# Performance work log

Hardware: AMD Instinct MI355X
Metric: run time of the kernel (lower is better)

## Reference

```python
import jax, jax.numpy as jnp
import numpy as np
import math

N = 1500; E = 24000; C_IN = 16; H = 64; NUM_LAYERS = 10; RATIO = 0.9
NEG = -1e9


def setup_inputs() -> dict:
    key = jax.random.key(0)
    ks = jax.random.split(key, 40)
    it = iter(range(40))
    def nrm(shape, scale=0.1):
        return jax.random.normal(ks[next(it)], shape, dtype=jnp.float32) * scale
    src = jax.random.randint(ks[next(it)], (E,), 0, N, dtype=jnp.int32)
    off = jax.random.randint(ks[next(it)], (E,), 1, N, dtype=jnp.int32)
    dst = (src + off) % N  # no self loops in the raw edge list
    return dict(
        x=nrm((N, C_IN), 1.0),
        edge_src=src, edge_dst=dst,
        W1=nrm((C_IN, H // 2)), b1=jnp.zeros((H // 2,), jnp.float32),
        W2=nrm((H // 2, H)), b2=jnp.zeros((H,), jnp.float32),
        W3=nrm((H, H)), b3=jnp.zeros((H,), jnp.float32),
        Wrel=nrm((NUM_LAYERS - 1, H, H)), brel=jnp.zeros((NUM_LAYERS - 1, H), jnp.float32),
        Wroot=nrm((NUM_LAYERS - 1, H, H)),
        pW=nrm((4, H, H)), pb=jnp.zeros((4, H), jnp.float32),
        leW1=nrm((4, H, 1)), leb1=jnp.zeros((4, 1), jnp.float32),
        leW2=nrm((4, H, 1)),
        leW3=nrm((4, H, 1)), leb3=jnp.zeros((4, 1), jnp.float32),
        linW1=nrm((NUM_LAYERS * H, H)), linb1=jnp.zeros((H,), jnp.float32),
        linW2=nrm((H, 10)), linb2=jnp.zeros((10,), jnp.float32),
    )


def _seg_mean(vals, idx, n):
    s = jax.ops.segment_sum(vals, idx, num_segments=n)
    c = jax.ops.segment_sum(jnp.ones((idx.shape[0],), vals.dtype), idx, num_segments=n)
    return s / jnp.maximum(c, 1.0)[:, None]


def _feast(x, W, b, srcL, dstL, n):
    # FeaStConv with heads=1: softmax over a single head == 1 -> mean of lin(x_j) + bias
    return _seg_mean((x @ W)[srcL], dstL, n) + b


def _gconv_sparse(x, src, dst, Wr, br, Wo, n):
    return _seg_mean(x[src], dst, n) @ Wr + br + x @ Wo


def _gconv_dense(x, A, Wr, br, Wo):
    # mean aggregation: divide weighted sum by count of (nonzero) in-edges
    Mf = (A != 0).astype(x.dtype)
    agg = (A.T @ x) / jnp.maximum(Mf.sum(0), 1.0)[:, None]
    return agg @ Wr + br + x @ Wo


def _topk_pool(xc, fitness, ratio):
    k = int(math.ceil(ratio * xc.shape[0]))
    fit_k, perm = jax.lax.top_k(fitness, k)
    return xc[perm] * fit_k[:, None], perm


def _asap_sparse(x, src, dst, pW, pb, leW1, leb1, leW2, leW3, leb3):
    n = x.shape[0]
    ar = jnp.arange(n, dtype=src.dtype)
    srcL = jnp.concatenate([src, ar])  # add remaining self loops (weight 1)
    dstL = jnp.concatenate([dst, ar])
    xq = jax.ops.segment_max(x[srcL], dstL, num_segments=n) @ pW + pb
    s = jax.nn.leaky_relu(jnp.sum(xq[dstL] * x[srcL], -1), 0.2)
    m = jax.ops.segment_max(s, dstL, num_segments=n)
    e = jnp.exp(s - m[dstL])
    score = e / jax.ops.segment_sum(e, dstL, num_segments=n)[dstL]
    xc = jax.ops.segment_sum(x[srcL] * score[:, None], dstL, num_segments=n)
    # LEConv fitness score (edge weight = 1)
    a = xc @ leW1 + leb1
    b = xc @ leW2
    agg = jax.ops.segment_sum(a[srcL] - b[dstL], dstL, num_segments=n)
    fitness = jax.nn.sigmoid((agg + xc @ leW3 + leb3)[:, 0])
    x_new, perm = _topk_pool(xc, fitness, RATIO)
    S = jnp.zeros((n, n), x.dtype).at[srcL, dstL].add(score)
    A = jnp.zeros((n, n), x.dtype).at[srcL, dstL].add(1.0)
    Sp = S[:, perm]
    A_new = Sp.T @ A @ Sp
    k = A_new.shape[0]
    return x_new, A_new * (1.0 - jnp.eye(k, dtype=x.dtype))  # remove diag


def _asap_dense(x, A, pW, pb, leW1, leb1, leW2, leW3, leb3):
    n = x.shape[0]
    A = A + jnp.diag((jnp.diag(A) == 0).astype(A.dtype))  # add remaining self loops
    M = A != 0
    Mf = M.astype(x.dtype)
    xq = jnp.max(jnp.where(M[:, :, None], x[:, None, :], NEG), axis=0) @ pW + pb  # [n,H]
    Sc = jnp.where(M, jax.nn.leaky_relu(x @ xq.T, 0.2), NEG)  # [j,i]
    m = Sc.max(0)
    e = jnp.where(M, jnp.exp(Sc - m), 0.0)
    score = e / e.sum(0)
    xc = score.T @ x
    a = xc @ leW1 + leb1
    b = xc @ leW2
    agg = Mf.T @ a - Mf.sum(0)[:, None] * b
    fitness = jax.nn.sigmoid((agg + xc @ leW3 + leb3)[:, 0])
    x_new, perm = _topk_pool(xc, fitness, RATIO)
    Sp = score[:, perm]
    A_new = Sp.T @ A @ Sp
    k = A_new.shape[0]
    return x_new, A_new * (1.0 - jnp.eye(k, dtype=x.dtype))


def _forward(x, edge_src, edge_dst, W1, b1, W2, b2, W3, b3, Wrel, brel, Wroot,
             pW, pb, leW1, leb1, leW2, leW3, leb3, linW1, linb1, linW2, linb2):
    n = x.shape[0]
    ar = jnp.arange(n, dtype=edge_src.dtype)
    srcL = jnp.concatenate([edge_src, ar])  # FeaStConv add_self_loops=True
    dstL = jnp.concatenate([edge_dst, ar])
    x = jax.nn.elu(_feast(x, W1, b1, srcL, dstL, n))
    x = jax.nn.elu(_feast(x, W2, b2, srcL, dstL, n))
    x = jax.nn.elu(_feast(x, W3, b3, srcL, dstL, n))
    xs = [x.mean(0, keepdims=True)]  # single graph -> global_mean_pool == mean
    A = None
    for i in range(NUM_LAYERS - 1):
        if A is None:
            x = jax.nn.relu(_gconv_sparse(x, edge_src, edge_dst, Wrel[i], brel[i], Wroot[i], x.shape[0]))
        else:
            x = jax.nn.relu(_gconv_dense(x, A, Wrel[i], brel[i], Wroot[i]))
        xs.append(x.mean(0, keepdims=True))
        if i % 2 == 0 and i < NUM_LAYERS - 2:
            p = i // 2
            args = (pW[p], pb[p], leW1[p], leb1[p], leW2[p], leW3[p], leb3[p])
            if A is None:
                x, A = _asap_sparse(x, edge_src, edge_dst, *args)
            else:
                x, A = _asap_dense(x, A, *args)
    h = jnp.concatenate(xs, axis=-1)  # [1, NUM_LAYERS*H] jumping-knowledge cat
    h = jax.nn.relu(h @ linW1 + linb1)
    return jax.nn.log_softmax(h @ linW2 + linb2, axis=-1)


def reference(x, edge_src, edge_dst, W1, b1, W2, b2, W3, b3, Wrel, brel, Wroot,
              pW, pb, leW1, leb1, leW2, leW3, leb3, linW1, linb1, linW2, linb2):
    return _forward(x, edge_src, edge_dst, W1, b1, W2, b2, W3, b3, Wrel, brel, Wroot,
                    pW, pb, leW1, leb1, leW2, leW3, leb3, linW1, linb1, linW2, linb2)
```

## Files before the change

kernel.cpp:

```cpp
#include <hip/hip_runtime.h>
#include <math.h>

#define NEGV -1000000000.0f

typedef short short8 __attribute__((ext_vector_type(8)));
typedef float floatx4 __attribute__((ext_vector_type(4)));

__device__ __forceinline__ float sigm(float x){ return 1.0f/(1.0f+expf(-x)); }
__device__ __forceinline__ void edge_sd(int e,const int* src,const int* dst,int E,int& s,int& d){
  if(e<E){ s=src[e]; d=dst[e]; } else { s=e-E; d=s; }
}
__device__ __forceinline__ ushort bf16rn(float x){
  unsigned u = __float_as_uint(x);
  unsigned r = (u + 0x7fffu + ((u>>16)&1u)) >> 16;
  return (ushort)r;
}
__device__ __forceinline__ float bf16f(ushort h){ return __uint_as_float(((unsigned)h)<<16); }

__global__ void k_zero(float* __restrict__ p, size_t n){
  size_t i = (size_t)blockIdx.x*256 + threadIdx.x;
  if (i < n) p[i] = 0.0f;
}
__global__ void k_fillm1(int* __restrict__ p, int n){
  int i = blockIdx.x*256 + threadIdx.x;
  if (i < n) p[i] = -1;
}
__global__ void k_ipos(const int* __restrict__ perm, int* __restrict__ ipos, int kk){
  int p = blockIdx.x*256 + threadIdx.x;
  if (p < kk) ipos[perm[p]] = p;
}
__global__ void k_prep2(const int* __restrict__ rowD,const int* __restrict__ eidD,
                        const float* __restrict__ scE,int2* __restrict__ Mt,int L2,int kk){
  int p = blockIdx.x*256+threadIdx.x; if(p>=L2) return;
  Mt[p] = make_int2(rowD[p]*kk, __float_as_int(scE[eidD[p]]));
}

__global__ void k_split3(const float* __restrict__ src,int R,int Cs,int ld,
                         ushort* __restrict__ dst,int Cp,int bmode){
  int idx = blockIdx.x*256+threadIdx.x;
  if (idx >= R*Cp) return;
  int r = idx / Cp, c = idx - r*Cp;
  float x = (c < Cs) ? src[(size_t)r*ld + c] : 0.0f;
  ushort h = bf16rn(x);
  ushort l = bf16rn(x - bf16f(h));
  size_t base = (size_t)r*(3*Cp) + c;
  dst[base]        = h;
  dst[base + Cp]   = bmode ? l : h;
  dst[base + 2*Cp] = bmode ? h : l;
}
__global__ void k_split3_Tdual(const float* __restrict__ src,int Rs,int Cs,int ld,
                               const int* __restrict__ gperm,const float* __restrict__ cscale,
                               const float* __restrict__ emax,
                               ushort* __restrict__ dstA,ushort* __restrict__ dstB,
                               ushort* __restrict__ dstCpad,int Kp){
  __shared__ float t[32][33];
  int tx = threadIdx.x & 31, ty = threadIdx.x >> 5;
  int kb = blockIdx.y*32, xb = blockIdx.x*32;
  int x = xb + tx;
  int gx = (x < Cs) ? gperm[x] : 0;
#pragma unroll
  for (int i=0;i<4;i++){
    int k = kb + ty + i*8;
    t[ty+i*8][tx] = (k < Rs && x < Cs) ? src[(size_t)k*ld + gx] : 0.0f;
  }
  __syncthreads();
  const int K3 = 3*Kp;
#pragma unroll
  for (int i=0;i<4;i++){
    int xo = xb + ty + i*8, ko = kb + tx;
    if (xo < Cs){
      float v = 0.0f;
      if (ko < Rs){
        int g = gperm[xo];
        v = expf(t[tx][ty+i*8] - emax[g]) * cscale[g];
      }
      ushort h = bf16rn(v);
      ushort l = bf16rn(v - bf16f(h));
      size_t base = (size_t)xo*K3 + ko;
      dstA[base] = h; dstA[base+Kp] = h; dstA[base+2*Kp] = l;
      dstB[base] = h; dstB[base+Kp] = l; dstB[base+2*Kp] = h;
      if (ko >= Rs){ dstCpad[base]=0; dstCpad[base+Kp]=0; dstCpad[base+2*Kp]=0; }
    }
  }
}

template<int EPI>
__global__ __launch_bounds__(256) void k_gemm_mfma(
    const ushort* __restrict__ A, const ushort* __restrict__ B,
    float* __restrict__ C, int ldc, int M, int N, int K3,
    const float* __restrict__ mask, int ldm)
{
  __shared__ ushort As[2][64][72];
  __shared__ ushort Bs[2][64][72];
  const int tid = threadIdx.x;
  const int m0 = blockIdx.y*64, n0 = blockIdx.x*64;
  const int w = tid>>6, lane = tid&63;
  const int lo4 = lane&15, quad = lane>>4;
  const int sr = tid>>2, sseg = tid&3;

  floatx4 acc[4];
#pragma unroll
  for(int c=0;c<4;c++){ acc[c][0]=0.f; acc[c][1]=0.f; acc[c][2]=0.f; acc[c][3]=0.f; }

  const size_t arow = (size_t)(m0+sr)*K3;
  const size_t brow = (size_t)(n0+sr)*K3;
  const bool aval = (m0+sr) < M;
  const bool bval = (n0+sr) < N;

  uint4 av0 = make_uint4(0,0,0,0), av1 = make_uint4(0,0,0,0);
  uint4 bv0 = make_uint4(0,0,0,0), bv1 = make_uint4(0,0,0,0);
  if (aval){ av0 = *(const uint4*)(A + arow + sseg*8);
             av1 = *(const uint4*)(A + arow + 32 + sseg*8); }
  if (bval){ bv0 = *(const uint4*)(B + brow + sseg*8);
             bv1 = *(const uint4*)(B + brow + 32 + sseg*8); }
  *(uint4*)&As[0][sr][sseg*8] = av0; *(uint4*)&As[0][sr][32+sseg*8] = av1;
  *(uint4*)&Bs[0][sr][sseg*8] = bv0; *(uint4*)&Bs[0][sr][32+sseg*8] = bv1;
  __syncthreads();

  const int T = K3 >> 6;
  for (int i=0;i<T;i++){
    const int cb = i & 1;
    if (i+1 < T){
      const int k0 = (i+1)<<6;
      av0 = make_uint4(0,0,0,0); av1 = make_uint4(0,0,0,0);
      bv0 = make_uint4(0,0,0,0); bv1 = make_uint4(0,0,0,0);
      if (aval){ av0 = *(const uint4*)(A + arow + k0 + sseg*8);
                 av1 = *(const uint4*)(A + arow + k0 + 32 + sseg*8); }
      if (bval){ bv0 = *(const uint4*)(B + brow + k0 + sseg*8);
                 bv1 = *(const uint4*)(B + brow + k0 + 32 + sseg*8); }
    }
    short8 af0 = *(const short8*)&As[cb][16*w + lo4][quad*8];
    short8 af1 = *(const short8*)&As[cb][16*w + lo4][32+quad*8];
#pragma unroll
    for (int c=0;c<4;c++){
      short8 bf0 = *(const short8*)&Bs[cb][16*c + lo4][quad*8];
      acc[c] = __builtin_amdgcn_mfma_f32_16x16x32_bf16(af0, bf0, acc[c], 0, 0, 0);
      short8 bf1 = *(const short8*)&Bs[cb][16*c + lo4][32+quad*8];
      acc[c] = __builtin_amdgcn_mfma_f32_16x16x32_bf16(af1, bf1, acc[c], 0, 0, 0);
    }
    if (i+1 < T){
      __syncthreads();
      *(uint4*)&As[1-cb][sr][sseg*8] = av0; *(uint4*)&As[1-cb][sr][32+sseg*8] = av1;
      *(uint4*)&Bs[1-cb][sr][sseg*8] = bv0; *(uint4*)&Bs[1-cb][sr][32+sseg*8] = bv1;
      __syncthreads();
    }
  }

#pragma unroll
  for (int c=0;c<4;c++){
    const int gn = n0 + 16*c + lo4;
#pragma unroll
    for (int r=0;r<4;r++){
      const int gm = m0 + 16*w + quad*4 + r;
      if (gm < M && gn < N){
        float v = acc[c][r];
        if (EPI==1) v = (mask[(size_t)gm*ldm+gn] != 0.0f || gm==gn) ? (v > 0.0f ? v : 0.2f*v) : NEGV;
        C[(size_t)gm*ldc+gn] = v;
      }
    }
  }
}

__global__ __launch_bounds__(256) void k_gemm_pp(
    const ushort* __restrict__ A, const ushort* __restrict__ B,
    float* __restrict__ P0, float* __restrict__ P1,
    float* __restrict__ P2, float* __restrict__ P3, int ldp,
    int M, int N, int K3, int kchunk)
{
  __shared__ ushort As[2][128][72];
  __shared__ ushort Bs[2][128][72];
  const int tid = threadIdx.x;
  const int m0 = blockIdx.y*128, n0 = blockIdx.x*128;
  const int w = tid>>6, lane = tid&63;
  const int lo4 = lane&15, quad = lane>>4;
  const int wr = w>>1, wc = w&1;

  const int srow = tid>>1, shalf = tid&1;

  const int z = blockIdx.z;
  float* __restrict__ P = (z==0) ? P0 : (z==1) ? P1 : (z==2) ? P2 : P3;
  const int kbeg = z * kchunk;
  int klen = K3 - kbeg; if (klen > kchunk) klen = kchunk; if (klen < 0) klen = 0;
  const int T = klen >> 6;

  floatx4 acc[4][4];
#pragma unroll
  for(int i=0;i<4;i++)
#pragma unroll
    for(int c=0;c<4;c++){ acc[i][c][0]=0.f; acc[i][c][1]=0.f; acc[i][c][2]=0.f; acc[i][c][3]=0.f; }

  const size_t arow = (size_t)(m0+srow)*K3 + kbeg + shalf*32;
  const size_t brow = (size_t)(n0+srow)*K3 + kbeg + shalf*32;
  const bool aval = (m0+srow) < M;
  const bool bval = (n0+srow) < N;
  const int sbase = shalf*32;

  uint4 apre[4], bpre[4];
#pragma unroll
  for(int s=0;s<4;s++){ apre[s]=make_uint4(0,0,0,0); bpre[s]=make_uint4(0,0,0,0); }
  if (aval){
#pragma unroll
    for(int s=0;s<4;s++) apre[s] = *(const uint4*)(A + arow + s*8);
  }
  if (bval){
#pragma unroll
    for(int s=0;s<4;s++) bpre[s] = *(const uint4*)(B + brow + s*8);
  }
#pragma unroll
  for(int s=0;s<4;s++){
    *(uint4*)&As[0][srow][sbase + s*8] = apre[s];
    *(uint4*)&Bs[0][srow][sbase + s*8] = bpre[s];
  }
  __syncthreads();

  for (int it=0; it<T; ++it){
    const int cb = it & 1;
    if (it+1 < T){
      const int k0 = (it+1)<<6;
#pragma unroll
      for(int s=0;s<4;s++){ apre[s]=make_uint4(0,0,0,0); bpre[s]=make_uint4(0,0,0,0); }
      if (aval){
#pragma unroll
        for(int s=0;s<4;s++) apre[s] = *(const uint4*)(A + arow + k0 + s*8);
      }
      if (bval){
#pragma unroll
        for(int s=0;s<4;s++) bpre[s] = *(const uint4*)(B + brow + k0 + s*8);
      }
    }
    short8 af[4][2];
#pragma unroll
    for(int i=0;i<4;i++){
      af[i][0] = *(const short8*)&As[cb][wr*64 + 16*i + lo4][quad*8];
      af[i][1] = *(const short8*)&As[cb][wr*64 + 16*i + lo4][32 + quad*8];
    }
#pragma unroll
    for(int c=0;c<4;c++){
      short8 bf0 = *(const short8*)&Bs[cb][wc*64 + 16*c + lo4][quad*8];
      short8 bf1 = *(const short8*)&Bs[cb][wc*64 + 16*c + lo4][32 + quad*8];
#pragma unroll
      for(int i=0;i<4;i++){
        acc[i][c] = __builtin_amdgcn_mfma_f32_16x16x32_bf16(af[i][0], bf0, acc[i][c], 0, 0, 0);
        acc[i][c] = __builtin_amdgcn_mfma_f32_16x16x32_bf16(af[i][1], bf1, acc[i][c], 0, 0, 0);
      }
    }
    if (it+1 < T){
      __syncthreads();
#pragma unroll
      for(int s=0;s<4;s++){
        *(uint4*)&As[1-cb][srow][sbase + s*8] = apre[s];
        *(uint4*)&Bs[1-cb][srow][sbase + s*8] = bpre[s];
      }
      __syncthreads();
    }
  }

#pragma unroll
  for(int c=0;c<4;c++){
    const int gn = n0 + wc*64 + 16*c + lo4;
    if (gn < N){
#pragma unroll
      for(int i=0;i<4;i++){
#pragma unroll
        for(int r=0;r<4;r++){
          const int gm = m0 + wr*64 + 16*i + quad*4 + r;
          if (gm < M) P[(size_t)gm*ldp+gn] = acc[i][c][r];
        }
      }
    }
  }
}

__global__ __launch_bounds__(256) void k_red_tb(
    const float* __restrict__ P0,const float* __restrict__ P1,
    const float* __restrict__ P2,const float* __restrict__ P3,int ldp,
    const ushort* __restrict__ Bb, ushort* __restrict__ Cb,
    int M,int N,int Kp)
{
  __shared__ float t[32][33];
  const int tx = threadIdx.x & 31, ty = threadIdx.x >> 5;
  const int mb = blockIdx.y*32, nb = blockIdx.x*32;
  const int n = nb + tx;
#pragma unroll
  for (int i=0;i<4;i++){
    int m = mb + ty + i*8;
    float v = 0.0f;
    if (m < M && n < N){
      size_t o = (size_t)m*ldp + n;
      v = (P0[o] + P1[o]) + (P2[o] + P3[o]);
    }
    t[ty+i*8][tx] = v;
  }
  __syncthreads();
  const int K3o = 3*Kp;
#pragma unroll
  for (int i=0;i<4;i++){
    int no = nb + ty + i*8, mo = mb + tx;
    if (no < N && mo < M){
      size_t base = (size_t)no*K3o + mo;
      float sp = bf16f(Bb[base]) + bf16f(Bb[base+Kp]);
      float v = t[tx][ty+i*8] + sp;
      ushort h = bf16rn(v), l = bf16rn(v - bf16f(h));
      Cb[base] = h; Cb[base+Kp] = l; Cb[base+2*Kp] = h;
    }
  }
}

__global__ void k_red_diag(const float* __restrict__ P0,const float* __restrict__ P1,
                           const float* __restrict__ P2,const float* __restrict__ P3,
                           float* __restrict__ C,int kk){
  int idx = blockIdx.x*256+threadIdx.x;
  if (idx >= kk*kk) return;
  int u = idx/kk, v = idx - u*kk;
  float s = (P0[idx] + P1[idx]) + (P2[idx] + P3[idx]);
  C[idx] = (u==v) ? 0.0f : s;
}

template<bool MAXM, bool COUNT, bool EXPM, bool SELF>
__global__ __launch_bounds__(256) void k_skinny(
    const float* __restrict__ A, int lda,
    const float* __restrict__ X,
    const float* __restrict__ mcol,
    float* __restrict__ P, int* __restrict__ cntp,
    int M, int K, int kchunk)
{
  __shared__ float As[16][68];
  __shared__ float Xs[16][68];
  const int tid = threadIdx.x;
  const int m0 = blockIdx.y * 64;
  const int tmb = (tid & 15) * 4, tnb = (tid >> 4) * 4;
  float acc[4][4];
  int cacc[4] = {0,0,0,0};
#pragma unroll
  for (int i=0;i<4;i++)
#pragma unroll
    for (int j=0;j<4;j++) acc[i][j] = MAXM ? NEGV : 0.0f;

  const int kstart = blockIdx.z * kchunk;
  int kend = kstart + kchunk; if (kend > K) kend = K;
  const int ml = tid & 63, tb = tid >> 6;
  const bool mvalid = (m0 + ml) < M;
  float mc = 0.0f;
  if (EXPM && mvalid) mc = mcol[m0 + ml];

  for (int k0 = kstart; k0 < kend; k0 += 16) {
#pragma unroll
    for (int s=0;s<4;s++) {
      const int tk = tb + s*4;
      float va = 0.0f, vx = 0.0f;
      if ((k0+tk) < K) {
        if (mvalid){
          va = A[(size_t)(k0+tk)*lda + m0 + ml];
          if (EXPM) va = expf(va - mc);
        }
        vx = X[(size_t)(k0+tk)*64 + ml];
      }
      As[tk][ml] = va;
      Xs[tk][ml] = vx;
    }
    __syncthreads();
#pragma unroll
    for (int kk=0; kk<16; kk++) {
      const float4 a4 = *(const float4*)&As[kk][tmb];
      const float4 b4 = *(const float4*)&Xs[kk][tnb];
      const float av[4] = {a4.x,a4.y,a4.z,a4.w};
      const float bv[4] = {b4.x,b4.y,b4.z,b4.w};
#pragma unroll
      for (int i=0;i<4;i++){
        if (COUNT) cacc[i] += (av[i] != 0.0f) ? 1 : 0;
#pragma unroll
        for (int j=0;j<4;j++) {
          if (MAXM) acc[i][j] = fmaxf(acc[i][j], av[i] != 0.0f ? bv[j] : NEGV);
          else      acc[i][j] = fmaf(av[i], bv[j], acc[i][j]);
        }
      }
    }
    __syncthreads();
  }

  const size_t slab = (size_t)blockIdx.z * M * 64;
#pragma unroll
  for (int i=0;i<4;i++){
    const int m = m0 + tmb + i;
    if (m < M){
#pragma unroll
      for (int j=0;j<4;j++){
        float v = acc[i][j];
        if (SELF) v = fmaxf(v, X[(size_t)m*64 + tnb + j]);
        P[slab + (size_t)m*64 + tnb + j] = v;
      }
    }
  }
  if (COUNT && tnb == 0){
#pragma unroll
    for (int i=0;i<4;i++){
      const int m = m0 + tmb + i;
      if (m < M) cntp[blockIdx.z*M + m] = cacc[i];
    }
  }
}

__global__ __launch_bounds__(256) void k_poolq(
    const float* __restrict__ SEGP,const int* __restrict__ cntp8,int Z,
    const float* __restrict__ pWp,const float* __restrict__ pbp,
    const float* __restrict__ X,
    ushort* __restrict__ dstA,ushort* __restrict__ dstB,
    float* __restrict__ cntP,int n)
{
  __shared__ float xq[4][65];
  const int tid = threadIdx.x;
  const int r = tid>>6, j = tid&63;
  const int i = blockIdx.x*4 + r;
  float v = NEGV;
  if (i < n){
    for(int z=0;z<Z;z++) v = fmaxf(v, SEGP[(size_t)z*n*64 + (size_t)i*64 + j]);
    if (j == 0){
      int c=1; for(int z=0;z<Z;z++) c += cntp8[z*n+i];
      cntP[i] = (float)c;
    }
  }
  xq[r][j] = v;
  __syncthreads();
  if (i < n){
    float s = pbp[j];
    for(int q=0;q<64;q++) s = fmaf(xq[r][q], pWp[q*64+j], s);
    size_t base = (size_t)i*192 + j;
    ushort h = bf16rn(s), l = bf16rn(s - bf16f(h));
    dstB[base] = h; dstB[base+64] = l; dstB[base+128] = h;
    float x = X[(size_t)i*64 + j];
    h = bf16rn(x); l = bf16rn(x - bf16f(h));
    dstA[base] = h; dstA[base+64] = h; dstA[base+128] = l;
  }
}

__global__ __launch_bounds__(256) void k_gconv_fuse(
    const float* __restrict__ SEGP,const int* __restrict__ cntp8,int Z,
    const float* __restrict__ Wrel,const float* __restrict__ brel,
    const float* __restrict__ X,const float* __restrict__ Wroot,
    float* __restrict__ XN,int n,float* __restrict__ meanacc,float inv_n)
{
  __shared__ float agg_s[4][65];
  __shared__ float xrow[4][65];
  __shared__ float cnt_s[4];
  const int tid = threadIdx.x;
  const int r = tid>>6, j = tid&63;
  const int i = blockIdx.x*4 + r;
  float a = 0.0f;
  if (i < n){
    for(int z=0;z<Z;z++) a += SEGP[(size_t)z*n*64 + (size_t)i*64 + j];
    xrow[r][j] = X[(size_t)i*64 + j];
    if (j == 0){
      int c=0; for(int z=0;z<Z;z++) c += cntp8[z*n+i];
      cnt_s[r] = (float)(c>1?c:1);
    }
  }
  agg_s[r][j] = a;
  __syncthreads();
  float v = 0.0f;
  if (i < n){
    float acc=0.0f, rt=0.0f;
    for(int q=0;q<64;q++){
      acc = fmaf(agg_s[r][q], Wrel[q*64+j], acc);
      rt  = fmaf(xrow[r][q],  Wroot[q*64+j], rt);
    }
    v = fmaxf(acc/cnt_s[r] + brel[j] + rt, 0.0f);
    XN[(size_t)i*64 + j] = v;
  }
  __syncthreads();
  agg_s[r][j] = v;
  __syncthreads();
  if (r == 0) atomicAdd(&meanacc[j], (agg_s[0][j]+agg_s[1][j]+agg_s[2][j]+agg_s[3][j])*inv_n);
}

__global__ __launch_bounds__(256) void k_smax_fused(const float* __restrict__ S,int n,
                                                    float* __restrict__ mcol,float* __restrict__ invd){
  __shared__ float red[16][17];
  const int jc = threadIdx.x & 15, rg = threadIdx.x >> 4;
  const int j = blockIdx.x*16 + jc;
  float m = -3.0e38f;
  if (j < n)
    for(int i=rg;i<n;i+=16) m = fmaxf(m, S[(size_t)i*n+j]);
  red[rg][jc] = m;
  __syncthreads();
  for(int s=8;s>0;s>>=1){
    if(rg<s) red[rg][jc] = fmaxf(red[rg][jc], red[rg+s][jc]);
    __syncthreads();
  }
  const float mc = red[0][jc];
  __syncthreads();
  float sum = 0.0f;
  if (j < n)
    for(int i=rg;i<n;i+=16) sum += expf(S[(size_t)i*n+j]-mc);
  red[rg][jc] = sum;
  __syncthreads();
  for(int s=8;s>0;s>>=1){
    if(rg<s) red[rg][jc] += red[rg+s][jc];
    __syncthreads();
  }
  if(rg==0 && j<n){ mcol[j]=mc; invd[j]=1.0f/red[0][jc]; }
}

__global__ __launch_bounds__(256) void k_xcabc_dense(
    const float* __restrict__ SEGP,int Z,const float* __restrict__ invd,
    float* __restrict__ XC,
    const float* __restrict__ w1,const float* bb1,const float* __restrict__ w2,
    const float* __restrict__ w3,const float* bb3,
    float* aN,float* bN,float* cN,int* pcnt,int n)
{
  __shared__ float xc[4][65];
  const int tid = threadIdx.x;
  const int r = tid>>6, j = tid&63;
  const int i = blockIdx.x*4 + r;
  if (blockIdx.x==0 && tid==0) *pcnt = 0;
  float v = 0.0f;
  if (i < n){
    for(int z=0;z<Z;z++) v += SEGP[(size_t)z*n*64 + (size_t)i*64 + j];
    v *= invd[i];
    XC[(size_t)i*64+j] = v;
  }
  xc[r][j] = v;
  __syncthreads();
  if (i < n && j < 3){
    float s = (j==0)?bb1[0]:((j==2)?bb3[0]:0.0f);
    const float* w = (j==0)?w1:((j==1)?w2:w3);
    for(int q=0;q<64;q++) s = fmaf(xc[r][q], w[q], s);
    if(j==0) aN[i]=s; else if(j==1) bN[i]=s; else cN[i]=s;
  }
}

__global__ void k_aggcol(const float* __restrict__ A,const float* __restrict__ aN,
                         float* __restrict__ aggp,int n){
  int idx = blockIdx.x*256+threadIdx.x; if(idx>=n*16) return;
  int j = idx % n, c = idx / n;
  int i0 = (int)(((long long)n*c)/16), i1 = (int)(((long long)n*(c+1))/16);
  float s = 0.0f;
  for(int i=i0;i<i1;i++) if(A[(size_t)i*n + j] != 0.0f) s += aN[i];
  aggp[c*n + j] = s;
}

__global__ void k_fit_dense(const float* __restrict__ aggp,const float* __restrict__ cntP,
                            const float* __restrict__ aN,const float* __restrict__ bN,
                            const float* __restrict__ cN,
                            float* __restrict__ fit,int* __restrict__ rank,int* pcnt,int n){
  int u = blockIdx.x*256+threadIdx.x;
  if (blockIdx.x==0 && threadIdx.x==0) *pcnt = 0;
  if (u >= n) return;
  float a = aN[u];
  for(int c=0;c<16;c++) a += aggp[c*n+u];
  fit[u] = sigm(a - cntP[u]*bN[u] + cN[u]);
  rank[u] = 0;
}
__global__ __launch_bounds__(256) void k_rank_cnt(const float* __restrict__ fit,
                                                  int* __restrict__ rank,int n){
  __shared__ float fsc[128];
  const int u0 = blockIdx.y*128;
  int u1 = u0+128; if (u1 > n) u1 = n;
  const int cl = u1 - u0;
  if ((int)threadIdx.x < cl) fsc[threadIdx.x] = fit[u0+threadIdx.x];
  __syncthreads();
  const int v = blockIdx.x*256+threadIdx.x;
  if (v >= n) return;
  const float fv = fit[v];
  int r = 0;
  for(int t=0;t<cl;t++){
    const float fu = fsc[t];
    const int u = u0+t;
    r += (fu > fv || (fu == fv && u < v)) ? 1 : 0;
  }
  atomicAdd(&rank[v], r);
}
__global__ __launch_bounds__(256) void k_rank_sel(const int* __restrict__ rank,
    const float* __restrict__ fit,const float* __restrict__ XC,float* __restrict__ XN,
    int n,int k,int* pcnt,int* perm){
  __shared__ int ps[4];
  const int r = threadIdx.x>>6, h = threadIdx.x&63;
  const int v = blockIdx.x*4 + r;
  const bool sel = (v < n) && (rank[v] < k);
  if (h == 0 && sel){
    int p = atomicAdd(pcnt,1);
    ps[r] = p;
    perm[p] = v;
  }
  __syncthreads();
  if (sel){
    const int p = ps[r];
    XN[(size_t)p*64 + h] = XC[(size_t)v*64 + h] * fit[v];
  }
}

__global__ void k_deg(const int* __restrict__ src,const int* __restrict__ dst,int* indeg,int* outdeg,int E){
  int e = blockIdx.x*256+threadIdx.x; if(e>=E) return;
  atomicAdd(&indeg[dst[e]],1); atomicAdd(&outdeg[src[e]],1);
}
__global__ __launch_bounds__(256) void k_prefix2(const int* __restrict__ indeg,const int* __restrict__ outdeg,
                          int* offD,int* curD,int* offS,int* curS,int n){
  __shared__ int ds[1504];
  const int* dsrc = blockIdx.y ? outdeg : indeg;
  for(int u=threadIdx.x; u<n; u+=256) ds[u] = dsrc[u];
  __syncthreads();
  int t = blockIdx.x*256+threadIdx.x; if(t>n) return;
  int s = 0;
  for(int u=0;u<t;u++) s += ds[u]+1;
  if (blockIdx.y){ offS[t]=s; if(t<n) curS[t]=s; }
  else           { offD[t]=s; if(t<n) curD[t]=s; }
}
__global__ void k_csr_fill2(const int* src,const int* dst,
                            int* curS,int* colS,int* eidS,
                            int* curD,int* rowD,int* eidD,int E,int n){
  int e = blockIdx.x*256+threadIdx.x; if(e>=E+n) return;
  int s,d; edge_sd(e,src,dst,E,s,d);
  int p = atomicAdd(&curS[s],1); colS[p]=d; eidS[p]=e;
  int q = atomicAdd(&curD[d],1); rowD[q]=s; eidD[q]=e;
}

__global__ void k_mm_small(const float* __restrict__ A,const float* __restrict__ W,
                           const float* __restrict__ b,float* __restrict__ C,
                           int M,int K,int Np,int act){
  int idx = blockIdx.x*256+threadIdx.x; if(idx>=M*Np) return;
  int m = idx/Np, j = idx - m*Np;
  float s = b ? b[j] : 0.0f;
  const float* a = A + (size_t)m*K;
  for(int q=0;q<K;q++) s = fmaf(a[q], W[(size_t)q*Np + j], s);
  if(act==1) s = fmaxf(s, 0.0f);
  C[idx] = s;
}

__global__ void k_feast_gf(const float* __restrict__ Y,const int* __restrict__ offD,
                           const int* __restrict__ rowD,
                           const float* __restrict__ b,float* X,int n,int H,
                           float* __restrict__ meanacc,float inv_n){
  __shared__ float ms[4][64];
  int idx = blockIdx.x*256+threadIdx.x;
  float v = 0.0f;
  if(idx<n*H){
    int i = idx/H, h = idx - i*H;
    int p0 = offD[i], p1 = offD[i+1];
    float s = 0.0f;
    for(int p=p0;p<p1;p++) s += Y[(size_t)rowD[p]*H + h];
    float t = s/(float)(p1-p0) + b[h];
    v = t > 0.0f ? t : (expf(t)-1.0f);
    X[idx] = v;
  }
  if(meanacc){
    int r = threadIdx.x>>6, j = threadIdx.x&63;
    ms[r][j] = (idx<n*H) ? v : 0.0f;
    __syncthreads();
    if(r==0) atomicAdd(&meanacc[j], (ms[0][j]+ms[1][j]+ms[2][j]+ms[3][j])*inv_n);
  }
}

__global__ __launch_bounds__(256) void k_gconv_sparse_f(
    const float* __restrict__ X,const int* __restrict__ offD,const int* __restrict__ rowD,
    const int* __restrict__ eidD,int E,
    const float* __restrict__ Wrel,const float* __restrict__ brel,
    const float* __restrict__ Wroot,
    float* __restrict__ XN,int n,float* __restrict__ meanacc,float inv_n)
{
  __shared__ float agg_s[4][65];
  __shared__ float xrow[4][65];
  __shared__ float cnt_s[4];
  const int tid = threadIdx.x;
  const int r = tid>>6, j = tid&63;
  const int i = blockIdx.x*4 + r;
  float a = 0.0f;
  if (i < n){
    int p0 = offD[i], p1 = offD[i+1], c = 0;
    for(int p=p0;p<p1;p++){
      if (eidD[p] < E){ a += X[(size_t)rowD[p]*64 + j]; c++; }
    }
    xrow[r][j] = X[(size_t)i*64 + j];
    if (j == 0) cnt_s[r] = (float)(c>1?c:1);
  }
  agg_s[r][j] = a;
  __syncthreads();
  float v = 0.0f;
  if (i < n){
    float acc=0.0f, rt=0.0f;
    for(int q=0;q<64;q++){
      acc = fmaf(agg_s[r][q], Wrel[q*64+j], acc);
      rt  = fmaf(xrow[r][q],  Wroot[q*64+j], rt);
    }
    v = fmaxf(acc/cnt_s[r] + brel[j] + rt, 0.0f);
    XN[(size_t)i*64 + j] = v;
  }
  __syncthreads();
  agg_s[r][j] = v;
  __syncthreads();
  if (r == 0) atomicAdd(&meanacc[j], (agg_s[0][j]+agg_s[1][j]+agg_s[2][j]+agg_s[3][j])*inv_n);
}

__global__ __launch_bounds__(256) void k_xqmaxq(
    const float* __restrict__ X,const int* __restrict__ offD,const int* __restrict__ rowD,
    const float* __restrict__ pWp,const float* __restrict__ pbp,
    float* __restrict__ XQ2,int n)
{
  __shared__ float xq[4][65];
  const int tid = threadIdx.x;
  const int r = tid>>6, j = tid&63;
  const int i = blockIdx.x*4 + r;
  float v = -3.0e38f;
  if (i < n){
    int p0 = offD[i], p1 = offD[i+1];
    for(int p=p0;p<p1;p++) v = fmaxf(v, X[(size_t)rowD[p]*64 + j]);
  }
  xq[r][j] = v;
  __syncthreads();
  if (i < n){
    float s = pbp[j];
    for(int q=0;q<64;q++) s = fmaf(xq[r][q], pWp[q*64+j], s);
    XQ2[(size_t)i*64+j] = s;
  }
}

__global__ void k_edge_score(const int* __restrict__ src,const int* __restrict__ dst,
                             const float* __restrict__ XQ2,const float* __restrict__ X,
                             float* sE,int E,int n){
  int e = blockIdx.x*256+threadIdx.x; if(e>=E+n) return;
  int s,d; edge_sd(e,src,dst,E,s,d);
  const float* q = XQ2 + (size_t)d*64;
  const float* x = X + (size_t)s*64;
  float acc = 0.0f;
  for(int h=0;h<64;h++) acc = fmaf(q[h], x[h], acc);
  sE[e] = acc > 0.0f ? acc : 0.2f*acc;
}

__global__ void k_dstsoft(const int* __restrict__ offD,const int* __restrict__ eidD,
                          const float* __restrict__ sE,float* __restrict__ scE,int n){
  int i = blockIdx.x*256+threadIdx.x; if(i>=n) return;
  int p0 = offD[i], p1 = offD[i+1];
  float m = -3.0e38f;
  for(int p=p0;p<p1;p++) m = fmaxf(m, sE[eidD[p]]);
  float d = 0.0f;
  for(int p=p0;p<p1;p++) d += expf(sE[eidD[p]]-m);
  float inv = 1.0f/d;
  for(int p=p0;p<p1;p++){ int e = eidD[p]; scE[e] = expf(sE[e]-m)*inv; }
}

__global__ __launch_bounds__(256) void k_xcabc0(
    const int* __restrict__ offD,const int* __restrict__ rowD,const int* __restrict__ eidD,
    const float* __restrict__ scE,const float* __restrict__ X,
    float* __restrict__ XC,
    const float* __restrict__ w1,const float* bb1,const float* __restrict__ w2,
    const float* __restrict__ w3,const float* bb3,
    float* aN,float* bN,float* cN,int* pcnt,int n)
{
  __shared__ float xc[4][65];
  const int tid = threadIdx.x;
  const int r = tid>>6, j = tid&63;
  const int i = blockIdx.x*4 + r;
  if (blockIdx.x==0 && tid==0) *pcnt = 0;
  float v = 0.0f;
  if (i < n){
    int p0 = offD[i], p1 = offD[i+1];
    for(int p=p0;p<p1;p++) v += scE[eidD[p]] * X[(size_t)rowD[p]*64 + j];
    XC[(size_t)i*64+j] = v;
  }
  xc[r][j] = v;
  __syncthreads();
  if (i < n && j < 3){
    float s = (j==0)?bb1[0]:((j==2)?bb3[0]:0.0f);
    const float* w = (j==0)?w1:((j==1)?w2:w3);
    for(int q=0;q<64;q++) s = fmaf(xc[r][q], w[q], s);
    if(j==0) aN[i]=s; else if(j==1) bN[i]=s; else cN[i]=s;
  }
}

__global__ void k_aggfit0(const int* __restrict__ offD,const int* __restrict__ rowD,
                          const float* aN,const float* bN,const float* cN,
                          float* fit,int* __restrict__ rank,int n){
  int i = blockIdx.x*256+threadIdx.x; if(i>=n) return;
  int p0 = offD[i], p1 = offD[i+1];
  float s = 0.0f;
  for(int p=p0;p<p1;p++) s += aN[rowD[p]];
  fit[i] = sigm(s - (float)(p1-p0)*bN[i] + cN[i]);
  rank[i] = 0;
}

__global__ void k_stage1p(const int* src,const int* dst,const int* __restrict__ offS,
                          const int* __restrict__ colS,const int* __restrict__ eidS,
                          const float* __restrict__ scE,const int* __restrict__ ipos,
                          float* Rp,int E,int n,int kk){
  int e = blockIdx.x*256+threadIdx.x; if(e>=E+n) return;
  int i,j; edge_sd(e,src,dst,E,i,j);
  int p0 = offS[j], p1 = offS[j+1];
  float* Ri = Rp + (size_t)i*kk;
  for(int p=p0;p<p1;p++){
    int ip = ipos[colS[p]];
    if (ip >= 0) atomicAdd(&Ri[ip], scE[eidS[p]]);
  }
}
__global__ __launch_bounds__(256) void k_stage2x(
    const int* __restrict__ perm,const int* __restrict__ offD,
    const int2* __restrict__ Mt,
    const float* __restrict__ Rp,float* A,int k,int vw,int cbn){
  const int bid = blockIdx.x;
  const int slice = bid & 7;
  const int rest = bid >> 3;
  const int cb = rest % cbn;
  const int ub = rest / cbn;
  const int u = ub*4 + (threadIdx.x>>6);
  if (u >= k) return;
  const int vbase = slice*vw;
  int vend = vbase + vw; if (vend > k) vend = k;
  const int v = vbase + cb*64 + (threadIdx.x&63);
  const bool vok = v < vend;
  const int vs = vok ? v : vbase;
  const int d = perm[u];
  float acc = 0.0f;
  int p = offD[d];
  const int p1 = offD[d+1];
  for(; p+4 <= p1; p += 4){
    const int2 m0 = Mt[p];
    const int2 m1 = Mt[p+1];
    const int2 m2 = Mt[p+2];
    const int2 m3 = Mt[p+3];
    const float r0 = Rp[m0.x + vs];
    const float r1 = Rp[m1.x + vs];
    const float r2 = Rp[m2.x + vs];
    const float r3 = Rp[m3.x + vs];
    acc = fmaf(__int_as_float(m0.y), r0, acc);
    acc = fmaf(__int_as_float(m1.y), r1, acc);
    acc = fmaf(__int_as_float(m2.y), r2, acc);
    acc = fmaf(__int_as_float(m3.y), r3, acc);
  }
  for(; p < p1; ++p){
    const int2 m = Mt[p];
    acc = fmaf(__int_as_float(m.y), Rp[m.x + vs], acc);
  }
  if (vok) A[(size_t)u*k + v] = (u==v) ? 0.0f : acc;
}

__global__ void k_head2(const float* __restrict__ xs,const float* __restrict__ W1,
                        const float* __restrict__ b1,const float* __restrict__ W2,
                        const float* __restrict__ b2,float* out){
  __shared__ float h2[64];
  __shared__ float lg[10];
  int t = threadIdx.x;
  float s = b1[t];
  for(int q=0;q<640;q++) s = fmaf(xs[q], W1[q*64+t], s);
  h2[t] = fmaxf(s, 0.0f);
  __syncthreads();
  if(t < 10){
    float s2 = b2[t];
    for(int k=0;k<64;k++) s2 = fmaf(h2[k], W2[k*10+t], s2);
    lg[t] = s2;
  }
  __syncthreads();
  if(t == 0){
    float mx = lg[0];
    for(int i=1;i<10;i++) mx = fmaxf(mx, lg[i]);
    float se = 0.0f;
    for(int i=0;i<10;i++) se += expf(lg[i]-mx);
    float lse = mx + logf(se);
    for(int i=0;i<10;i++) out[i] = lg[i]-lse;
  }
}

extern "C" void kernel_launch(void* const* d_in, const int* in_sizes, int n_in,
                              void* d_out, int out_size, void* d_ws, size_t ws_size,
                              hipStream_t stream) {
  const int N0 = 1500, E = 24000, Z = 16, L = E + N0;
  const float* x0   = (const float*)d_in[0];
  const int* esrc   = (const int*)d_in[1];
  const int* edst   = (const int*)d_in[2];
  const float* W1   = (const float*)d_in[3];  const float* b1   = (const float*)d_in[4];
  const float* W2   = (const float*)d_in[5];  const float* b2   = (const float*)d_in[6];
  const float* W3   = (const float*)d_in[7];  const float* b3   = (const float*)d_in[8];
  const float* Wrel = (const float*)d_in[9];  const float* brel = (const float*)d_in[10];
  const float* Wroot= (const float*)d_in[11];
  const float* pW   = (const float*)d_in[12]; const float* pb   = (const float*)d_in[13];
  const float* leW1 = (const float*)d_in[14]; const float* leb1 = (const float*)d_in[15];
  const float* leW2 = (const float*)d_in[16]; const float* leW3 = (const float*)d_in[17];
  const float* leb3 = (const float*)d_in[18];
  const float* linW1= (const float*)d_in[19]; const float* linb1= (const float*)d_in[20];
  const float* linW2= (const float*)d_in[21]; const float* linb2= (const float*)d_in[22];
  float* out = (float*)d_out;

  float* ws = (float*)d_ws;
  size_t cur = 0;
  auto allocF = [&](size_t nf)->float*{ float* p = ws + cur; cur += (nf + 15) & ~(size_t)15; return p; };
  float* xs   = allocF(640);
  int* indeg  = (int*)allocF(1504);
  int* outdeg = (int*)allocF(1504);
  float* Xa  = allocF(96000); float* Xb  = allocF(96000); float* Y   = allocF(96000);
  float* XQ2 = allocF(96000); float* XC  = allocF(96000);
  float* mcol = allocF(1504); float* invd = allocF(1504);
  float* aN = allocF(1504); float* bN = allocF(1504); float* cN = allocF(1504);
  float* fit = allocF(1504); float* cntP = allocF(1504);
  int* pcnt = (int*)allocF(16);
  int* perm = (int*)allocF(1504);
  int* offD = (int*)allocF(1504); int* offS = (int*)allocF(1504);
  int* curD = (int*)allocF(1504); int* curS = (int*)allocF(1504);
  int* colS = (int*)allocF(25504); int* eidS = (int*)allocF(25504);
  int* rowD = (int*)allocF(25504); int* eidD = (int*)allocF(25504);
  float* sE = allocF(25504); float* scE = allocF(25504);
  int2* Mt  = (int2*)allocF(51008);
  int* cntp8 = (int*)allocF((size_t)Z*1504);
  float* aggp = allocF(16*1504);
  float* SEGP = allocF((size_t)Z*1504*64);
  float* Rbig = allocF((size_t)1500*1500);
  float* SCb  = Rbig;
  float* A0  = allocF((size_t)1350*1350);
  float* A1s = allocF((size_t)1350*1350);
  const size_t SLAB = 1650048;
  float* PS2 = allocF(SLAB);
  float* PS3 = allocF(SLAB);
  const size_t BFSZ = (size_t)1350*4224/2 + 32;
  ushort* Abf = (ushort*)allocF(BFSZ);
  ushort* Bbf = (ushort*)allocF(BFSZ);
  ushort* Cbf = (ushort*)allocF(BFSZ);
  ushort* Dbf = (ushort*)allocF(BFSZ);
  int* rankb = indeg;

  dim3 B256(256);
  auto G1 = [&](size_t n){ return dim3((unsigned)((n + 255) / 256)); };
  auto ZF = [&](void* p, size_t nfloats){ k_zero<<<G1(nfloats),B256,0,stream>>>((float*)p, nfloats); };
  auto kcz = [&](int K){ return (int)(((K + Z*16 - 1) / (Z*16)) * 16); };

  ZF(xs, 640 + 1504 + 1504);
  k_deg<<<G1(E),B256,0,stream>>>(esrc, edst, indeg, outdeg, E);
  k_prefix2<<<dim3((N0+256)/256,2),B256,0,stream>>>(indeg, outdeg, offD, curD, offS, curS, N0);
  k_csr_fill2<<<G1(L),B256,0,stream>>>(esrc, edst, curS, colS, eidS, curD, rowD, eidD, E, N0);

  auto feast = [&](const float* xin,int cin,const float* W,const float* bb,int hh,float* xout,float* macc){
    k_mm_small<<<G1((size_t)N0*hh),B256,0,stream>>>(xin, W, nullptr, Y, N0, cin, hh, 0);
    k_feast_gf<<<G1((size_t)N0*hh),B256,0,stream>>>(Y, offD, rowD, bb, xout, N0, hh, macc, 1.0f/N0);
  };
  feast(x0, 16, W1, b1, 32, Xa, nullptr);
  feast(Xa, 32, W2, b2, 64, Xb, nullptr);
  feast(Xb, 64, W3, b3, 64, Xa, xs + 0);
  float* X = Xa; float* XN = Xb;

  k_gconv_sparse_f<<<dim3((N0+3)/4),B256,0,stream>>>(X, offD, rowD, eidD, E, Wrel, brel, Wroot,
                                                     XN, N0, xs + 64, 1.0f/N0);
  { float* t = X; X = XN; XN = t; }

  {
    const int n = 1500, kk = 1350;
    k_xqmaxq<<<dim3((n+3)/4),B256,0,stream>>>(X, offD, rowD, pW, pb, XQ2, n);
    k_edge_score<<<G1(L),B256,0,stream>>>(esrc, edst, XQ2, X, sE, E, n);
    k_dstsoft<<<G1(n),B256,0,stream>>>(offD, eidD, sE, scE, n);
    k_prep2<<<G1(L),B256,0,stream>>>(rowD, eidD, scE, Mt, L, kk);
    k_xcabc0<<<dim3((n+3)/4),B256,0,stream>>>(offD, rowD, eidD, scE, X, XC,
                                              leW1, leb1, leW2, leW3, leb3, aN, bN, cN, pcnt, n);
    k_aggfit0<<<G1(n),B256,0,stream>>>(offD, rowD, aN, bN, cN, fit, rankb, n);
    k_rank_cnt<<<dim3((n+255)/256,(n+127)/128),B256,0,stream>>>(fit, rankb, n);
    k_rank_sel<<<dim3((n+3)/4),B256,0,stream>>>(rankb, fit, XC, XN, n, kk, pcnt, perm);
    int* ipos = curD;
    k_fillm1<<<G1(n),B256,0,stream>>>(ipos, n);
    k_ipos<<<G1(kk),B256,0,stream>>>(perm, ipos, kk);
    ZF(Rbig, (size_t)n*kk);
    k_stage1p<<<G1(L),B256,0,stream>>>(esrc, edst, offS, colS, eidS, scE, ipos, Rbig, E, n, kk);
    {
      const int vw = (kk + 7) / 8;
      const int cbn = (vw + 63) / 64;
      const int ubn = (kk + 3) / 4;
      k_stage2x<<<dim3((unsigned)(8*cbn*ubn)),B256,0,stream>>>(perm, offD, Mt,
                                                               Rbig, A0, kk, vw, cbn);
    }
    { float* t = X; X = XN; XN = t; }
  }

  float* Acur = A0; float* Aoth = A1s;
  int nn = 1350;

  auto gconv_dense = [&](int layer){
    dim3 g(1, (nn+63)/64, Z);
    k_skinny<false,true,false,false><<<g,B256,0,stream>>>(Acur, nn, X, nullptr, SEGP, cntp8, nn, nn, kcz(nn));
    k_gconv_fuse<<<dim3((nn+3)/4),B256,0,stream>>>(SEGP, cntp8, Z,
        Wrel + (size_t)layer*4096, brel + layer*64, X, Wroot + (size_t)layer*4096,
        XN, nn, xs + (size_t)(layer+1)*64, 1.0f/nn);
    { float* t = X; X = XN; XN = t; }
  };

  auto asap_dense = [&](int kk, int p){
    {
      dim3 g(1, (nn+63)/64, Z);
      k_skinny<true,true,false,true><<<g,B256,0,stream>>>(Acur, nn, X, nullptr, SEGP, cntp8, nn, nn, kcz(nn));
    }
    k_poolq<<<dim3((nn+3)/4),B256,0,stream>>>(SEGP, cntp8, Z, pW + (size_t)p*4096, pb + p*64,
                                              X, Abf, Bbf, cntP, nn);
    {
      dim3 g((nn+63)/64, (nn+63)/64);
      k_gemm_mfma<1><<<g,B256,0,stream>>>(Abf, Bbf, SCb, nn, nn, nn, 192, Acur, nn);
    }
    k_smax_fused<<<dim3((nn+15)/16),B256,0,stream>>>(SCb, nn, mcol, invd);
    {
      dim3 g(1, (nn+63)/64, Z);
      k_skinny<false,false,true,false><<<g,B256,0,stream>>>(SCb, nn, X, mcol, SEGP, nullptr, nn, nn, kcz(nn));
    }
    k_xcabc_dense<<<dim3((nn+3)/4),B256,0,stream>>>(SEGP, Z, invd, XC,
        leW1 + p*64, leb1 + p, leW2 + p*64, leW3 + p*64, leb3 + p, aN, bN, cN, pcnt, nn);
    k_aggcol<<<G1((size_t)nn*16),B256,0,stream>>>(Acur, aN, aggp, nn);
    k_fit_dense<<<G1(nn),B256,0,stream>>>(aggp, cntP, aN, bN, cN, fit, rankb, pcnt, nn);
    k_rank_cnt<<<dim3((nn+255)/256,(nn+127)/128),B256,0,stream>>>(fit, rankb, nn);
    k_rank_sel<<<dim3((nn+3)/4),B256,0,stream>>>(rankb, fit, XC, XN, nn, kk, pcnt, perm);
    const int Kp = (nn + 63) & ~63;
    const int K3 = 3*Kp;
    k_split3<<<G1((size_t)nn*Kp),B256,0,stream>>>(Acur, nn, nn, nn, Abf, Kp, 0);
    { dim3 gt((kk+31)/32, Kp/32);
      k_split3_Tdual<<<gt,B256,0,stream>>>(SCb, nn, kk, nn, perm, invd, mcol, Dbf, Bbf, Cbf, Kp); }
    const int Tk = K3 >> 6;
    const int kchunk = ((Tk + 3) >> 2) << 6;
    {
      dim3 g((kk+127)/128, (nn+127)/128, 4);
      k_gemm_pp<<<g,B256,0,stream>>>(Abf, Bbf, Rbig, Aoth, PS2, PS3, kk, nn, kk, K3, kchunk);
      dim3 gr((kk+31)/32, (nn+31)/32);
      k_red_tb<<<gr,B256,0,stream>>>(Rbig, Aoth, PS2, PS3, kk, Bbf, Cbf, nn, kk, Kp);
    }
    {
      dim3 g((kk+127)/128, (kk+127)/128, 4);
      k_gemm_pp<<<g,B256,0,stream>>>(Dbf, Cbf, Rbig, Aoth, PS2, PS3, kk, kk, kk, K3, kchunk);
      k_red_diag<<<G1((size_t)kk*kk),B256,0,stream>>>(Rbig, Aoth, PS2, PS3, Aoth, kk);
    }
    { float* t = X; X = XN; XN = t; }
    { float* t = Acur; Acur = Aoth; Aoth = t; }
    nn = kk;
  };

  gconv_dense(1);
  gconv_dense(2);
  asap_dense(1215, 1);
  gconv_dense(3);
  gconv_dense(4);
  asap_dense(1094, 2);
  gconv_dense(5);
  gconv_dense(6);
  asap_dense(985, 3);
  gconv_dense(7);
  gconv_dense(8);

  k_head2<<<1,64,0,stream>>>(xs, linW1, linb1, linW2, linb2, out);
}
```

Baseline: 1.354 ms.

## Fold small prep kernels into neighbors and remap gemm_pp blocks across XCDs

Removes three tiny launches: k_prep2 is folded into k_dstsoft, and k_fillm1/k_ipos are folded into k_aggfit0 and k_rank_sel, which now also writes the inverse permutation. The split-K gemm_pp kernel remaps its linear block ID so that consecutive tiles and the same K-chunk land on the same XCD (8-way round robin), aiming for better L2 reuse. The cost is some index arithmetic per block. Ordering stays correct because ipos is reset before rank_sel writes it.

```diff
diff --git a/kernel.cpp b/kernel.cpp
--- a/kernel.cpp
+++ b/kernel.cpp
@@ -20,19 +20,6 @@
 __global__ void k_zero(float* __restrict__ p, size_t n){
   size_t i = (size_t)blockIdx.x*256 + threadIdx.x;
   if (i < n) p[i] = 0.0f;
-}
-__global__ void k_fillm1(int* __restrict__ p, int n){
-  int i = blockIdx.x*256 + threadIdx.x;
-  if (i < n) p[i] = -1;
-}
-__global__ void k_ipos(const int* __restrict__ perm, int* __restrict__ ipos, int kk){
-  int p = blockIdx.x*256 + threadIdx.x;
-  if (p < kk) ipos[perm[p]] = p;
-}
-__global__ void k_prep2(const int* __restrict__ rowD,const int* __restrict__ eidD,
-                        const float* __restrict__ scE,int2* __restrict__ Mt,int L2,int kk){
-  int p = blockIdx.x*256+threadIdx.x; if(p>=L2) return;
-  Mt[p] = make_int2(rowD[p]*kk, __float_as_int(scE[eidD[p]]));
 }
 
 __global__ void k_split3(const float* __restrict__ src,int R,int Cs,int ld,
@@ -170,14 +157,24 @@
   __shared__ ushort As[2][128][72];
   __shared__ ushort Bs[2][128][72];
   const int tid = threadIdx.x;
-  const int m0 = blockIdx.y*128, n0 = blockIdx.x*128;
+
+  const int gx = gridDim.x, gxy = gridDim.x*gridDim.y;
+  const int TT = gxy*gridDim.z;
+  const int s  = blockIdx.x + gx*blockIdx.y + gxy*blockIdx.z;
+  const int c8 = s & 7, u = s >> 3;
+  const int q = TT >> 3, r8 = TT & 7;
+  const int w0 = (c8 < r8) ? c8*(q+1) + u : r8*(q+1) + (c8 - r8)*q + u;
+  const int z  = w0 / gxy;
+  const int lin = w0 - z*gxy;
+  const int ty = lin / gx, tx = lin - ty*gx;
+
+  const int m0 = ty*128, n0 = tx*128;
   const int w = tid>>6, lane = tid&63;
   const int lo4 = lane&15, quad = lane>>4;
   const int wr = w>>1, wc = w&1;
 
   const int srow = tid>>1, shalf = tid&1;
 
-  const int z = blockIdx.z;
   float* __restrict__ P = (z==0) ? P0 : (z==1) ? P1 : (z==2) ? P2 : P3;
   const int kbeg = z * kchunk;
   int klen = K3 - kbeg; if (klen > kchunk) klen = kchunk; if (klen < 0) klen = 0;
@@ -197,19 +194,19 @@
 
   uint4 apre[4], bpre[4];
 #pragma unroll
-  for(int s=0;s<4;s++){ apre[s]=make_uint4(0,0,0,0); bpre[s]=make_uint4(0,0,0,0); }
+  for(int s2=0;s2<4;s2++){ apre[s2]=make_uint4(0,0,0,0); bpre[s2]=make_uint4(0,0,0,0); }
   if (aval){
 #pragma unroll
-    for(int s=0;s<4;s++) apre[s] = *(const uint4*)(A + arow + s*8);
+    for(int s2=0;s2<4;s2++) apre[s2] = *(const uint4*)(A + arow + s2*8);
   }
   if (bval){
 #pragma unroll
-    for(int s=0;s<4;s++) bpre[s] = *(const uint4*)(B + brow + s*8);
-  }
-#pragma unroll
-  for(int s=0;s<4;s++){
-    *(uint4*)&As[0][srow][sbase + s*8] = apre[s];
-    *(uint4*)&Bs[0][srow][sbase + s*8] = bpre[s];
+    for(int s2=0;s2<4;s2++) bpre[s2] = *(const uint4*)(B + brow + s2*8);
+  }
+#pragma unroll
+  for(int s2=0;s2<4;s2++){
+    *(uint4*)&As[0][srow][sbase + s2*8] = apre[s2];
+    *(uint4*)&Bs[0][srow][sbase + s2*8] = bpre[s2];
   }
   __syncthreads();
 
@@ -218,14 +215,14 @@
     if (it+1 < T){
       const int k0 = (it+1)<<6;
 #pragma unroll
-      for(int s=0;s<4;s++){ apre[s]=make_uint4(0,0,0,0); bpre[s]=make_uint4(0,0,0,0); }
+      for(int s2=0;s2<4;s2++){ apre[s2]=make_uint4(0,0,0,0); bpre[s2]=make_uint4(0,0,0,0); }
       if (aval){
 #pragma unroll
-        for(int s=0;s<4;s++) apre[s] = *(const uint4*)(A + arow + k0 + s*8);
+        for(int s2=0;s2<4;s2++) apre[s2] = *(const uint4*)(A + arow + k0 + s2*8);
       }
       if (bval){
 #pragma unroll
-        for(int s=0;s<4;s++) bpre[s] = *(const uint4*)(B + brow + k0 + s*8);
+        for(int s2=0;s2<4;s2++) bpre[s2] = *(const uint4*)(B + brow + k0 + s2*8);
       }
     }
     short8 af[4][2];
@@ -247,9 +244,9 @@
     if (it+1 < T){
       __syncthreads();
 #pragma unroll
-      for(int s=0;s<4;s++){
-        *(uint4*)&As[1-cb][srow][sbase + s*8] = apre[s];
-        *(uint4*)&Bs[1-cb][srow][sbase + s*8] = bpre[s];
+      for(int s2=0;s2<4;s2++){
+        *(uint4*)&As[1-cb][srow][sbase + s2*8] = apre[s2];
+        *(uint4*)&Bs[1-cb][srow][sbase + s2*8] = bpre[s2];
       }
       __syncthreads();
     }
@@ -571,7 +568,7 @@
 }
 __global__ __launch_bounds__(256) void k_rank_sel(const int* __restrict__ rank,
     const float* __restrict__ fit,const float* __restrict__ XC,float* __restrict__ XN,
-    int n,int k,int* pcnt,int* perm){
+    int n,int k,int* pcnt,int* perm,int* __restrict__ ipos){
   __shared__ int ps[4];
   const int r = threadIdx.x>>6, h = threadIdx.x&63;
   const int v = blockIdx.x*4 + r;
@@ -580,6 +577,7 @@
     int p = atomicAdd(pcnt,1);
     ps[r] = p;
     perm[p] = v;
+    if (ipos) ipos[v] = p;
   }
   __syncthreads();
   if (sel){
@@ -725,7 +723,9 @@
 }
 
 __global__ void k_dstsoft(const int* __restrict__ offD,const int* __restrict__ eidD,
-                          const float* __restrict__ sE,float* __restrict__ scE,int n){
+                          const int* __restrict__ rowD,
+                          const float* __restrict__ sE,float* __restrict__ scE,
+                          int2* __restrict__ Mt,int kk,int n){
   int i = blockIdx.x*256+threadIdx.x; if(i>=n) return;
   int p0 = offD[i], p1 = offD[i+1];
   float m = -3.0e38f;
@@ -733,7 +733,12 @@
   float d = 0.0f;
   for(int p=p0;p<p1;p++) d += expf(sE[eidD[p]]-m);
   float inv = 1.0f/d;
-  for(int p=p0;p<p1;p++){ int e = eidD[p]; scE[e] = expf(sE[e]-m)*inv; }
+  for(int p=p0;p<p1;p++){
+    int e = eidD[p];
+    float v = expf(sE[e]-m)*inv;
+    scE[e] = v;
+    Mt[p] = make_int2(rowD[p]*kk, __float_as_int(v));
+  }
 }
 
 __global__ __launch_bounds__(256) void k_xcabc0(
@@ -767,13 +772,14 @@
 
 __global__ void k_aggfit0(const int* __restrict__ offD,const int* __restrict__ rowD,
                           const float* aN,const float* bN,const float* cN,
-                          float* fit,int* __restrict__ rank,int n){
+                          float* fit,int* __restrict__ rank,int* __restrict__ ipos,int n){
   int i = blockIdx.x*256+threadIdx.x; if(i>=n) return;
   int p0 = offD[i], p1 = offD[i+1];
   float s = 0.0f;
   for(int p=p0;p<p1;p++) s += aN[rowD[p]];
   fit[i] = sigm(s - (float)(p1-p0)*bN[i] + cN[i]);
   rank[i] = 0;
+  ipos[i] = -1;
 }
 
 __global__ void k_stage1p(const int* src,const int* dst,const int* __restrict__ offS,
@@ -937,18 +943,15 @@
 
   {
     const int n = 1500, kk = 1350;
+    int* ipos = curD;
     k_xqmaxq<<<dim3((n+3)/4),B256,0,stream>>>(X, offD, rowD, pW, pb, XQ2, n);
     k_edge_score<<<G1(L),B256,0,stream>>>(esrc, edst, XQ2, X, sE, E, n);
-    k_dstsoft<<<G1(n),B256,0,stream>>>(offD, eidD, sE, scE, n);
-    k_prep2<<<G1(L),B256,0,stream>>>(rowD, eidD, scE, Mt, L, kk);
+    k_dstsoft<<<G1(n),B256,0,stream>>>(offD, eidD, rowD, sE, scE, Mt, kk, n);
     k_xcabc0<<<dim3((n+3)/4),B256,0,stream>>>(offD, rowD, eidD, scE, X, XC,
                                               leW1, leb1, leW2, leW3, leb3, aN, bN, cN, pcnt, n);
-    k_aggfit0<<<G1(n),B256,0,stream>>>(offD, rowD, aN, bN, cN, fit, rankb, n);
+    k_aggfit0<<<G1(n),B256,0,stream>>>(offD, rowD, aN, bN, cN, fit, rankb, ipos, n);
     k_rank_cnt<<<dim3((n+255)/256,(n+127)/128),B256,0,stream>>>(fit, rankb, n);
-    k_rank_sel<<<dim3((n+3)/4),B256,0,stream>>>(rankb, fit, XC, XN, n, kk, pcnt, perm);
-    int* ipos = curD;
-    k_fillm1<<<G1(n),B256,0,stream>>>(ipos, n);
-    k_ipos<<<G1(kk),B256,0,stream>>>(perm, ipos, kk);
+    k_rank_sel<<<dim3((n+3)/4),B256,0,stream>>>(rankb, fit, XC, XN, n, kk, pcnt, perm, ipos);
     ZF(Rbig, (size_t)n*kk);
     k_stage1p<<<G1(L),B256,0,stream>>>(esrc, edst, offS, colS, eidS, scE, ipos, Rbig, E, n, kk);
     {
@@ -994,7 +997,7 @@
     k_aggcol<<<G1((size_t)nn*16),B256,0,stream>>>(Acur, aN, aggp, nn);
     k_fit_dense<<<G1(nn),B256,0,stream>>>(aggp, cntP, aN, bN, cN, fit, rankb, pcnt, nn);
     k_rank_cnt<<<dim3((nn+255)/256,(nn+127)/128),B256,0,stream>>>(fit, rankb, nn);
-    k_rank_sel<<<dim3((nn+3)/4),B256,0,stream>>>(rankb, fit, XC, XN, nn, kk, pcnt, perm);
+    k_rank_sel<<<dim3((nn+3)/4),B256,0,stream>>>(rankb, fit, XC, XN, nn, kk, pcnt, perm, nullptr);
     const int Kp = (nn + 63) & ~63;
     const int K3 = 3*Kp;
     k_split3<<<G1((size_t)nn*Kp),B256,0,stream>>>(Acur, nn, nn, nn, Abf, Kp, 0);
```

Result: no change. 1.347 ms, median of 2 (-0.5%).
